# Performance work log

Hardware: AMD Instinct MI355X
Metric: run time of the kernel (lower is better)

The kernel has to match this reference:

```python
import jax, jax.numpy as jnp
import numpy as np
import math

B, H, S, D = 2, 16, 2048, 64
NEG = -1000000000.0

def setup_inputs() -> dict:
    key = jax.random.key(0)
    kq, kk, kv, km = jax.random.split(key, 4)
    query = jax.random.normal(kq, (B, H, S, D), dtype=jnp.float32)
    k_ = jax.random.normal(kk, (B, H, S, D), dtype=jnp.float32)
    value = jax.random.normal(kv, (B, H, S, D), dtype=jnp.float32)
    mask = jax.random.randint(km, (B, 1, S, S), 0, 2, dtype=jnp.int32)
    return {"query": query, "key": k_, "value": value, "mask": mask}

def reference(query, key, value, mask):
    # scores: [B,H,S,S]
    scale = 1.0 / math.sqrt(query.shape[-1])
    scores = jnp.einsum('bhqd,bhkd->bhqk', query, key) * scale
    scores = jnp.where(mask == 0, NEG, scores)
    # NOTE: original code uses F.softmax(scores, dim=1) -> softmax over the
    # HEAD axis (axis=1) for 4D inputs. Reproduced faithfully.
    p_attn = jax.nn.softmax(scores, axis=1)
    out = jnp.einsum('bhqk,bhkd->bhqd', p_attn, value)
    return (out, p_attn)
```

## Files before the change

kernel.cpp:

```cpp
#include <hip/hip_runtime.h>
#include <hip/hip_bf16.h>
#include <stdint.h>

#define B_ 2
#define H_ 16
#define S_ 2048
#define D_ 64

typedef __attribute__((ext_vector_type(8))) short bf16x8;
typedef __attribute__((ext_vector_type(4))) float f32x4;

__device__ __forceinline__ short f2bf(float x){
  union { float f; uint32_t u; } v; v.f = x;
  uint32_t r = v.u + 0x7FFFu + ((v.u >> 16) & 1u);
  return (short)(r >> 16);
}

__device__ __forceinline__ int wfun(int x){ return (((x >> 2) << 1) | (x & 1)) & 7; }

__global__ __launch_bounds__(256) void cast_bf16(const float* __restrict__ X,
                                                 short* __restrict__ Y){
  size_t idx = ((size_t)blockIdx.x * 256 + threadIdx.x) * 8;
  float4 a = *(const float4*)(X + idx);
  float4 b = *(const float4*)(X + idx + 4);
  bf16x8 v;
  v[0]=f2bf(a.x); v[1]=f2bf(a.y); v[2]=f2bf(a.z); v[3]=f2bf(a.w);
  v[4]=f2bf(b.x); v[5]=f2bf(b.y); v[6]=f2bf(b.z); v[7]=f2bf(b.w);
  *(bf16x8*)(Y + idx) = v;
}

__global__ __launch_bounds__(256) void transpose_v(const float* __restrict__ V,
                                                   short* __restrict__ Vt){
  __shared__ float T[64][65];
  int bh = blockIdx.x >> 5;
  int k0 = (blockIdx.x & 31) * 64;
  int t = threadIdx.x;
  {
    int col = (t & 15) * 4;
    #pragma unroll
    for (int i = 0; i < 4; ++i){
      int row = (t >> 4) + i * 16;
      float4 a = *(const float4*)(V + ((size_t)bh * S_ + k0 + row) * D_ + col);
      T[col+0][row] = a.x; T[col+1][row] = a.y; T[col+2][row] = a.z; T[col+3][row] = a.w;
    }
  }
  __syncthreads();
  {
    int d  = t >> 2;
    int kk = (t & 3) * 16;
    bf16x8 o0, o1;
    #pragma unroll
    for (int j = 0; j < 8; ++j){
      o0[j] = f2bf(T[d][kk + j]);
      o1[j] = f2bf(T[d][kk + 8 + j]);
    }
    short* dst = Vt + ((size_t)bh * D_ + d) * S_ + k0 + kk;
    *(bf16x8*)(dst)     = o0;
    *(bf16x8*)(dst + 8) = o1;
  }
}

__global__ __launch_bounds__(256, 4) void pass1(const short* __restrict__ Qb,
                                                const short* __restrict__ Kb,
                                                const int* __restrict__ mask,
                                                float* __restrict__ Z){
  const int tid = threadIdx.x, w = tid >> 6, lane = tid & 63;
  const int g = lane >> 4, lr = lane & 15;
  const int bid = blockIdx.x;
  const int qg    = bid & 31;
  const int strip = (bid >> 5) & 15;
  const int b     = bid >> 9;
  const int q0 = qg * 64 + w * 16;
  const int ks = strip * 128;

  float dsum[8][4];
  #pragma unroll
  for (int st = 0; st < 8; ++st)
    #pragma unroll
    for (int r = 0; r < 4; ++r) dsum[st][r] = 0.f;

  for (int h = 0; h < 16; ++h){
    const size_t bh = (size_t)b * H_ + h;
    const short* qp = Qb + (bh * S_ + q0 + lr) * D_ + g * 8;
    bf16x8 qf0 = *(const bf16x8*)(qp);
    bf16x8 qf1 = *(const bf16x8*)(qp + 32);
    const short* kp = Kb + (bh * S_ + ks + lr) * D_ + g * 8;
    #pragma unroll 4
    for (int st = 0; st < 8; ++st){
      bf16x8 kf0 = *(const bf16x8*)(kp + (size_t)(st*16) * D_);
      bf16x8 kf1 = *(const bf16x8*)(kp + (size_t)(st*16) * D_ + 32);
      f32x4 s = (f32x4){0.f,0.f,0.f,0.f};
      s = __builtin_amdgcn_mfma_f32_16x16x32_bf16(qf0, kf0, s, 0, 0, 0);
      s = __builtin_amdgcn_mfma_f32_16x16x32_bf16(qf1, kf1, s, 0, 0, 0);
      #pragma unroll
      for (int r = 0; r < 4; ++r) dsum[st][r] += __expf(s[r] * 0.125f);
    }
  }

  #pragma unroll
  for (int st = 0; st < 8; ++st){
    #pragma unroll
    for (int r = 0; r < 4; ++r){
      const size_t qrow = (size_t)b * S_ + q0 + 4*g + r;
      const int kk = ks + st*16 + lr;
      int m = mask[qrow * S_ + kk];
      Z[qrow * S_ + kk] = m ? (1.0f / dsum[st][r]) : -1.0f;
    }
  }
}

__global__ __launch_bounds__(512, 4) void pass2(const short* __restrict__ Qb,
                                                const short* __restrict__ Kb,
                                                const short* __restrict__ Vt,
                                                const float* __restrict__ Z,
                                                float* __restrict__ out,
                                                float* __restrict__ pout){
  __shared__ short pl[8][16][64];

  const int tid = threadIdx.x, w = tid >> 6, lane = tid & 63;
  const int g = lane >> 4, lr = lane & 15;
  const int bid = blockIdx.x;
  const int strip = bid >> 5, b = (bid >> 4) & 1, h = bid & 15;
  const int q0 = strip * 128 + w * 16;
  const size_t bh = (size_t)b * 16 + h;

  bf16x8 qf0, qf1;
  {
    const short* qp = Qb + (bh * S_ + q0 + lr) * D_ + g * 8;
    qf0 = *(const bf16x8*)(qp);
    qf1 = *(const bf16x8*)(qp + 32);
  }

  f32x4 o[4];
  #pragma unroll
  for (int j = 0; j < 4; ++j) o[j] = (f32x4){0.f,0.f,0.f,0.f};

  const short* kb = Kb + (bh * S_ + lr) * D_ + g * 8;
  const short* vb = Vt + (bh * D_ + lr) * S_ + g * 8;
  const float* zl = Z    + ((size_t)b * S_ + q0 + 4*g) * S_ + lr;
  float*       pp = pout + (bh * S_ + q0 + 4*g) * S_ + lr;
  short*       plw = &pl[w][0][0];
  const int wl = wfun(lr);

  for (int it = 0; it < 32; ++it){
    const int k0 = it * 64;

    f32x4 zv[4];
    #pragma unroll
    for (int t = 0; t < 4; ++t)
      #pragma unroll
      for (int r = 0; r < 4; ++r)
        zv[t][r] = zl[(size_t)r * S_ + k0 + 16*t];

    f32x4 s[4];
    #pragma unroll
    for (int t = 0; t < 4; ++t){
      s[t] = (f32x4){0.f,0.f,0.f,0.f};
      bf16x8 kh0 = *(const bf16x8*)(kb + (size_t)(k0 + 16*t) * D_);
      bf16x8 kh1 = *(const bf16x8*)(kb + (size_t)(k0 + 16*t) * D_ + 32);
      s[t] = __builtin_amdgcn_mfma_f32_16x16x32_bf16(qf0, kh0, s[t], 0, 0, 0);
      s[t] = __builtin_amdgcn_mfma_f32_16x16x32_bf16(qf1, kh1, s[t], 0, 0, 0);
    }

    bf16x8 vr[4][2];
    #pragma unroll
    for (int j = 0; j < 4; ++j)
      #pragma unroll
      for (int m = 0; m < 2; ++m)
        vr[j][m] = *(const bf16x8*)(vb + (size_t)(16*j) * S_ + k0 + 32*m);

    #pragma unroll
    for (int t = 0; t < 4; ++t){
      #pragma unroll
      for (int r = 0; r < 4; ++r){
        float e = __expf(s[t][r] * 0.125f);
        float z = zv[t][r];
        float p = (z < 0.f) ? 0.0625f : e * z;
        pp[(size_t)r * S_ + k0 + 16*t] = p;
        int q = 4*g + r;
        int ksw = (16*t + lr) ^ (8 * wfun(q));
        plw[q*64 + ksw] = f2bf(p);
      }
    }

    bf16x8 pa0 = *(const bf16x8*)(plw + lr*64 + 8*( g      ^ wl));
    bf16x8 pa1 = *(const bf16x8*)(plw + lr*64 + 8*((4 + g) ^ wl));

    #pragma unroll
    for (int j = 0; j < 4; ++j){
      o[j] = __builtin_amdgcn_mfma_f32_16x16x32_bf16(pa0, vr[j][0], o[j], 0, 0, 0);
      o[j] = __builtin_amdgcn_mfma_f32_16x16x32_bf16(pa1, vr[j][1], o[j], 0, 0, 0);
    }
  }

  #pragma unroll
  for (int j = 0; j < 4; ++j)
    #pragma unroll
    for (int r = 0; r < 4; ++r)
      out[(bh * S_ + q0 + 4*g + r) * D_ + 16*j + lr] = o[j][r];
}

extern "C" void kernel_launch(void* const* d_in, const int* in_sizes, int n_in,
                              void* d_out, int out_size, void* d_ws, size_t ws_size,
                              hipStream_t stream){
  const float* Q    = (const float*)d_in[0];
  const float* K    = (const float*)d_in[1];
  const float* V    = (const float*)d_in[2];
  const int*   mask = (const int*)d_in[3];

  const size_t nkv = (size_t)B_ * H_ * S_ * D_;

  short* Qb  = (short*)d_ws;
  short* Kb  = Qb + nkv;
  short* Vt  = Kb + nkv;
  float* Zb  = (float*)(Vt + nkv);

  float* out  = (float*)d_out;
  float* pout = out + nkv;

  cast_bf16  <<<(int)(nkv / (256 * 8)), 256, 0, stream>>>(Q, Qb);
  cast_bf16  <<<(int)(nkv / (256 * 8)), 256, 0, stream>>>(K, Kb);
  transpose_v<<<B_ * H_ * (S_ / 64),    256, 0, stream>>>(V, Vt);
  pass1      <<<1024,                   256, 0, stream>>>(Qb, Kb, mask, Zb);
  pass2      <<<512,                    512, 0, stream>>>(Qb, Kb, Vt, Zb, out, pout);
}
```

Baseline: 513.1 us.

## Stage p_attn tiles in LDS and write them out as coalesced float4 rows

pass2 now keeps a 256-key-wide bf16 P tile per wave in shared memory and flushes it to the p_attn output as row-contiguous float4 stores. This replaces the scattered scalar 4-byte stores of the large probability matrix. K, V and Z loads are also grouped into a load phase, and the previous tile's flush is interleaved with the next tile's loads. The p_attn output is now rounded through bf16, which loses precision. LDS per block grows fourfold, to 64 KB, which can limit occupancy.

```diff
diff --git a/kernel.cpp b/kernel.cpp
--- a/kernel.cpp
+++ b/kernel.cpp
@@ -9,11 +9,16 @@
 
 typedef __attribute__((ext_vector_type(8))) short bf16x8;
 typedef __attribute__((ext_vector_type(4))) float f32x4;
+typedef __attribute__((ext_vector_type(4))) unsigned short u16x4;
 
 __device__ __forceinline__ short f2bf(float x){
   union { float f; uint32_t u; } v; v.f = x;
   uint32_t r = v.u + 0x7FFFu + ((v.u >> 16) & 1u);
   return (short)(r >> 16);
+}
+__device__ __forceinline__ float bf2f(short s){
+  union { uint32_t u; float f; } v; v.u = ((uint32_t)(uint16_t)s) << 16;
+  return v.f;
 }
 
 __device__ __forceinline__ int wfun(int x){ return (((x >> 2) << 1) | (x & 1)) & 7; }
@@ -115,7 +120,7 @@
                                                 const float* __restrict__ Z,
                                                 float* __restrict__ out,
                                                 float* __restrict__ pout){
-  __shared__ short pl[8][16][64];
+  __shared__ short pl[8][16][256];
 
   const int tid = threadIdx.x, w = tid >> 6, lane = tid & 63;
   const int g = lane >> 4, lr = lane & 15;
@@ -138,37 +143,40 @@
   const short* kb = Kb + (bh * S_ + lr) * D_ + g * 8;
   const short* vb = Vt + (bh * D_ + lr) * S_ + g * 8;
   const float* zl = Z    + ((size_t)b * S_ + q0 + 4*g) * S_ + lr;
-  float*       pp = pout + (bh * S_ + q0 + 4*g) * S_ + lr;
+  float*       prow = pout + (bh * S_ + q0) * S_;
   short*       plw = &pl[w][0][0];
-  const int wl = wfun(lr);
-
-  for (int it = 0; it < 32; ++it){
-    const int k0 = it * 64;
-
-    f32x4 zv[4];
+  const int wl8 = 8 * wfun(lr);
+
+  f32x4 zv[4];
+  bf16x8 kh[4][2];
+  bf16x8 vr[4][2];
+
+  auto load_all = [&](int k0){
     #pragma unroll
     for (int t = 0; t < 4; ++t)
       #pragma unroll
       for (int r = 0; r < 4; ++r)
         zv[t][r] = zl[(size_t)r * S_ + k0 + 16*t];
-
+    #pragma unroll
+    for (int t = 0; t < 4; ++t){
+      kh[t][0] = *(const bf16x8*)(kb + (size_t)(k0 + 16*t) * D_);
+      kh[t][1] = *(const bf16x8*)(kb + (size_t)(k0 + 16*t) * D_ + 32);
+    }
+    #pragma unroll
+    for (int j = 0; j < 4; ++j)
+      #pragma unroll
+      for (int m = 0; m < 2; ++m)
+        vr[j][m] = *(const bf16x8*)(vb + (size_t)(16*j) * S_ + k0 + 32*m);
+  };
+
+  auto compute = [&](int sub, int k0){
     f32x4 s[4];
     #pragma unroll
     for (int t = 0; t < 4; ++t){
       s[t] = (f32x4){0.f,0.f,0.f,0.f};
-      bf16x8 kh0 = *(const bf16x8*)(kb + (size_t)(k0 + 16*t) * D_);
-      bf16x8 kh1 = *(const bf16x8*)(kb + (size_t)(k0 + 16*t) * D_ + 32);
-      s[t] = __builtin_amdgcn_mfma_f32_16x16x32_bf16(qf0, kh0, s[t], 0, 0, 0);
-      s[t] = __builtin_amdgcn_mfma_f32_16x16x32_bf16(qf1, kh1, s[t], 0, 0, 0);
-    }
-
-    bf16x8 vr[4][2];
-    #pragma unroll
-    for (int j = 0; j < 4; ++j)
-      #pragma unroll
-      for (int m = 0; m < 2; ++m)
-        vr[j][m] = *(const bf16x8*)(vb + (size_t)(16*j) * S_ + k0 + 32*m);
-
+      s[t] = __builtin_amdgcn_mfma_f32_16x16x32_bf16(qf0, kh[t][0], s[t], 0, 0, 0);
+      s[t] = __builtin_amdgcn_mfma_f32_16x16x32_bf16(qf1, kh[t][1], s[t], 0, 0, 0);
+    }
     #pragma unroll
     for (int t = 0; t < 4; ++t){
       #pragma unroll
@@ -176,22 +184,44 @@
         float e = __expf(s[t][r] * 0.125f);
         float z = zv[t][r];
         float p = (z < 0.f) ? 0.0625f : e * z;
-        pp[(size_t)r * S_ + k0 + 16*t] = p;
         int q = 4*g + r;
-        int ksw = (16*t + lr) ^ (8 * wfun(q));
-        plw[q*64 + ksw] = f2bf(p);
+        int el = (sub*64 + 16*t + lr) ^ (8 * wfun(q));
+        plw[q*256 + el] = f2bf(p);
       }
     }
-
-    bf16x8 pa0 = *(const bf16x8*)(plw + lr*64 + 8*( g      ^ wl));
-    bf16x8 pa1 = *(const bf16x8*)(plw + lr*64 + 8*((4 + g) ^ wl));
-
+    bf16x8 pa0 = *(const bf16x8*)(plw + lr*256 + sub*64 + ((8*g)      ^ wl8));
+    bf16x8 pa1 = *(const bf16x8*)(plw + lr*256 + sub*64 + ((32 + 8*g) ^ wl8));
     #pragma unroll
     for (int j = 0; j < 4; ++j){
       o[j] = __builtin_amdgcn_mfma_f32_16x16x32_bf16(pa0, vr[j][0], o[j], 0, 0, 0);
       o[j] = __builtin_amdgcn_mfma_f32_16x16x32_bf16(pa1, vr[j][1], o[j], 0, 0, 0);
     }
-  }
+  };
+
+  auto flush = [&](int ps){
+    #pragma unroll
+    for (int row = 0; row < 16; ++row){
+      int el = (4*lane) ^ (8 * wfun(row));
+      u16x4 pb = *(const u16x4*)(plw + row*256 + el);
+      f32x4 pf;
+      #pragma unroll
+      for (int i = 0; i < 4; ++i) pf[i] = bf2f((short)pb[i]);
+      *(f32x4*)(prow + (size_t)row * S_ + ps*256 + 4*lane) = pf;
+    }
+  };
+
+  for (int sup = 0; sup < 8; ++sup){
+    const int kb0 = sup * 256;
+    load_all(kb0);
+    if (sup > 0) flush(sup - 1);
+    compute(0, kb0);
+    #pragma unroll
+    for (int sub = 1; sub < 4; ++sub){
+      load_all(kb0 + sub*64);
+      compute(sub, kb0 + sub*64);
+    }
+  }
+  flush(7);
 
   #pragma unroll
   for (int j = 0; j < 4; ++j)
```

New measurement: 554.5 us. 8.1% more time.
